# Optimization experiments

Hardware: AMD Instinct MI355X
Metric: run time of the kernel (lower is better)

## Reference

```python
import jax, jax.numpy as jnp
import numpy as np

B, D, H, W = 32, 256, 32, 32
K = 1024

def setup_inputs() -> dict:
    key = jax.random.key(0)
    k1, k2 = jax.random.split(key)
    x = jax.random.normal(k1, (B, D, H, W), dtype=jnp.float32)
    codebook = jax.random.normal(k2, (K, D), dtype=jnp.float32)
    return {"x": x, "codebook": codebook}

def reference(x, codebook):
    b, lat, h, w = x.shape
    # (B, D, H, W) -> (B*H*W, D) tokens
    xt = jnp.transpose(x, (0, 2, 3, 1)).reshape(-1, lat)  # [N, D]
    # Squared euclidean distances via expansion (argmin-equivalent to cdist)
    x_sq = jnp.sum(xt * xt, axis=-1, keepdims=True)           # [N, 1]
    c_sq = jnp.sum(codebook * codebook, axis=-1)[None, :]     # [1, K]
    dist2 = x_sq - 2.0 * (xt @ codebook.T) + c_sq             # [N, K]
    idx = jnp.argmin(dist2, axis=-1)                          # [N]
    quant = codebook[idx]                                     # [N, D]
    codebook_loss = jnp.mean((jax.lax.stop_gradient(xt) - quant) ** 2)
    commitment_loss = jnp.mean((xt - jax.lax.stop_gradient(quant)) ** 2)
    # Straight-through estimator
    out = xt + jax.lax.stop_gradient(quant - xt)              # [N, D]
    out = out.reshape(b, h, w, lat).transpose(0, 3, 1, 2)     # [B, D, H, W]
    min_enc_idx = idx.reshape(b, h, w)                        # [B, H, W]
    return out, min_enc_idx, codebook_loss, commitment_loss
```

## Files before the change

### kernel.cpp

```cpp
#include <hip/hip_runtime.h>

#define B_   32
#define D_   256
#define HW_  1024
#define N_   32768
#define K_   1024
#define DHW  (D_ * HW_)
#define MARGIN 0.3f

typedef __attribute__((ext_vector_type(8)))  short bf16x8;
typedef __attribute__((ext_vector_type(16))) float f32x16;

union FragU { uint4 q; bf16x8 v; };

__device__ inline uint bf16rne(float x) {
    uint ub = __float_as_uint(x);
    return (ub + 0x7fffu + ((ub >> 16) & 1u)) >> 16;
}

__global__ __launch_bounds__(256)
void prep_x(const float* __restrict__ x, uint4* __restrict__ xg) {
    const int tok0 = blockIdx.x * 64;
    const int b = tok0 >> 10, hw0 = tok0 & 1023;
    const int tokl = threadIdx.x & 63;
    const int gq = threadIdx.x >> 6;
    #pragma unroll
    for (int it = 0; it < 8; ++it) {
        int g = it * 4 + gq;
        const float* xp = x + (size_t)b * DHW + (size_t)(g * 8) * HW_ + hw0 + tokl;
        uint w[4];
        #pragma unroll
        for (int jj = 0; jj < 4; ++jj) {
            float e0 = xp[(size_t)(2 * jj) * HW_];
            float e1 = xp[(size_t)(2 * jj + 1) * HW_];
            w[jj] = bf16rne(e0) | (bf16rne(e1) << 16);
        }
        xg[(size_t)(tok0 + tokl) * 32 + g] = make_uint4(w[0], w[1], w[2], w[3]);
    }
}

__global__ __launch_bounds__(256)
void prep_cb(const float* __restrict__ cb, uint4* __restrict__ cbt,
             float* __restrict__ csq, float* __restrict__ cbT) {
    __shared__ uint sh[256], sl[256];
    __shared__ float rr[4];
    const int k = blockIdx.x, d = threadIdx.x;
    float v = cb[(size_t)k * D_ + d];
    uint hb = bf16rne(v);
    float hf = __uint_as_float(hb << 16);
    uint lb = bf16rne(v - hf);
    sh[d] = hb; sl[d] = lb;
    cbT[(size_t)d * K_ + k] = v;
    float s = v * v;
    #pragma unroll
    for (int off = 32; off >= 1; off >>= 1) s += __shfl_xor(s, off, 64);
    if ((d & 63) == 0) rr[d >> 6] = s;
    __syncthreads();
    if (d == 0) csq[k] = (rr[0] + rr[1]) + (rr[2] + rr[3]);
    if (d < 64) {
        int ch = d >> 3, g = d & 7;
        int p = g >> 2, gg = g & 3;
        const uint* src = p ? sl : sh;
        uint w[4];
        #pragma unroll
        for (int jj = 0; jj < 4; ++jj) {
            int dp = ch * 16 + gg * 4 + jj;
            w[jj] = src[2 * dp] | (src[2 * dp + 1] << 16);
        }
        cbt[(size_t)(ch * 1024 + k) * 8 + g] = make_uint4(w[0], w[1], w[2], w[3]);
    }
}

__global__ __launch_bounds__(512)
void vq_main(const uint4* __restrict__ xg, const uint4* __restrict__ cbt,
             const float* __restrict__ csqg, int* __restrict__ bestk,
             int* __restrict__ rcount, int* __restrict__ rlist,
             float* __restrict__ bdist) {
    __shared__ uint4 TkS[4096];
    __shared__ uint4 CbS[2][2048];
    __shared__ float csqS[1024];

    const int tid = threadIdx.x;
    const int lane = tid & 63;
    const int sub = lane >> 5, l31 = lane & 31;
    const int wid = tid >> 6;
    const int wm = wid >> 1, wn = wid & 1;
    const int tok0 = blockIdx.x * 128;

    csqS[tid] = csqg[tid];
    csqS[tid + 512] = csqg[tid + 512];
    asm volatile("s_waitcnt vmcnt(0) lgkmcnt(0)" ::: "memory");

    {
        const int tloc = tid >> 5;
        const int slot = tid & 31;
        const int g = slot ^ (tloc & 7);
        #pragma unroll
        for (int it = 0; it < 8; ++it) {
            int u = it * 512 + tid;
            const uint4* src = xg + (size_t)(tok0 + it * 16 + tloc) * 32 + g;
            __builtin_amdgcn_global_load_lds((const uint*)src, (uint*)&TkS[u], 16, 0, 0);
        }
    }
    const int s_cl = tid >> 3;
    const int s_g = (tid & 7) ^ (s_cl & 7);

    #pragma unroll
    for (int it = 0; it < 4; ++it) {
        int u = it * 512 + tid;
        int cl = it * 64 + s_cl;
        const uint4* src = cbt + (size_t)cl * 8 + s_g;
        __builtin_amdgcn_global_load_lds((const uint*)src, (uint*)&CbS[0][u], 16, 0, 0);
    }

    f32x16 acc[2][2] = {};
    float v1[2] = {3.4e38f, 3.4e38f}, v2[2] = {3.4e38f, 3.4e38f};
    int k1[2] = {0, 0};

    int cur = 0;
    for (int cc = 0; cc < 32; ++cc) {
        asm volatile("s_barrier" ::: "memory");
        if (cc + 1 < 32) {
            const int nct = (cc + 1) >> 3, nch = (cc + 1) & 7;
            #pragma unroll
            for (int it = 0; it < 4; ++it) {
                int u = it * 512 + tid;
                int cl = it * 64 + s_cl;
                const uint4* src = cbt + (size_t)(nch * 1024 + nct * 256 + cl) * 8 + s_g;
                __builtin_amdgcn_global_load_lds((const uint*)src, (uint*)&CbS[cur ^ 1][u], 16, 0, 0);
            }
            asm volatile("s_waitcnt vmcnt(4)" ::: "memory");
        } else {
            asm volatile("s_waitcnt vmcnt(0)" ::: "memory");
        }
        asm volatile("s_barrier" ::: "memory");

        const int ch = cc & 7;
        #pragma unroll
        for (int ks = 0; ks < 2; ++ks) {
            FragU tf[2], cfh[2], cfl[2];
            #pragma unroll
            for (int j = 0; j < 2; ++j) {
                int t = wn * 64 + j * 32 + l31;
                int g32 = ch * 4 + ks * 2 + sub;
                tf[j].q = TkS[t * 32 + (g32 ^ (t & 7))];
            }
            #pragma unroll
            for (int f = 0; f < 2; ++f) {
                int cl = wm * 64 + f * 32 + l31;
                int gh = ks * 2 + sub;
                int gl = 4 + ks * 2 + sub;
                cfh[f].q = CbS[cur][cl * 8 + (gh ^ (cl & 7))];
                cfl[f].q = CbS[cur][cl * 8 + (gl ^ (cl & 7))];
            }
            #pragma unroll
            for (int f = 0; f < 2; ++f)
                #pragma unroll
                for (int j = 0; j < 2; ++j) {
                    acc[f][j] = __builtin_amdgcn_mfma_f32_32x32x16_bf16(cfh[f].v, tf[j].v, acc[f][j], 0, 0, 0);
                    acc[f][j] = __builtin_amdgcn_mfma_f32_32x32x16_bf16(cfl[f].v, tf[j].v, acc[f][j], 0, 0, 0);
                }
        }
        cur ^= 1;

        if ((cc & 7) == 7) {
            const int ct = cc >> 3;
            const int cbase = ct * 256 + wm * 64 + sub * 4;
            #pragma unroll
            for (int f = 0; f < 2; ++f) {
                #pragma unroll
                for (int g8 = 0; g8 < 4; ++g8) {
                    float4 cs4 = *reinterpret_cast<const float4*>(&csqS[cbase + f * 32 + g8 * 8]);
                    const float csa[4] = {cs4.x, cs4.y, cs4.z, cs4.w};
                    #pragma unroll
                    for (int q = 0; q < 4; ++q) {
                        int code = cbase + f * 32 + g8 * 8 + q;
                        int r = g8 * 4 + q;
                        #pragma unroll
                        for (int j = 0; j < 2; ++j) {
                            float s = fmaf(-2.f, acc[f][j][r], csa[q]);
                            bool c = s < v1[j];
                            v2[j] = c ? v1[j] : fminf(v2[j], s);
                            k1[j] = c ? code : k1[j];
                            v1[j] = c ? s : v1[j];
                        }
                    }
                }
            }
            const f32x16 zf = {};
            #pragma unroll
            for (int f = 0; f < 2; ++f)
                #pragma unroll
                for (int j = 0; j < 2; ++j) acc[f][j] = zf;
        }
    }

    #pragma unroll
    for (int j = 0; j < 2; ++j) {
        float ov1 = __shfl_xor(v1[j], 32, 64);
        float ov2 = __shfl_xor(v2[j], 32, 64);
        int   ok1 = __shfl_xor(k1[j], 32, 64);
        float nv2 = fminf(fminf(v2[j], ov2), fmaxf(v1[j], ov1));
        if (ov1 < v1[j] || (ov1 == v1[j] && ok1 < k1[j])) { v1[j] = ov1; k1[j] = ok1; }
        v2[j] = nv2;
    }
    __syncthreads();
    float* red = (float*)&CbS[0][0];
    if (sub == 0) {
        #pragma unroll
        for (int j = 0; j < 2; ++j) {
            int t = wn * 64 + j * 32 + l31;
            red[(wm * 128 + t) * 4 + 0] = v1[j];
            red[(wm * 128 + t) * 4 + 1] = v2[j];
            red[(wm * 128 + t) * 4 + 2] = __int_as_float(k1[j]);
        }
    }
    __syncthreads();
    if (tid < 128) {
        float bv1 = red[tid * 4], bv2 = red[tid * 4 + 1];
        int bk = __float_as_int(red[tid * 4 + 2]);
        #pragma unroll
        for (int m = 1; m < 4; ++m) {
            float a1 = red[(m * 128 + tid) * 4], a2 = red[(m * 128 + tid) * 4 + 1];
            int ak = __float_as_int(red[(m * 128 + tid) * 4 + 2]);
            float nv2 = fminf(fminf(bv2, a2), fmaxf(bv1, a1));
            if (a1 < bv1 || (a1 == bv1 && ak < bk)) { bv1 = a1; bk = ak; }
            bv2 = nv2;
        }
        int n = tok0 + tid;
        bestk[n] = bk;
        bdist[n] = bv1;
        if (bv2 - bv1 < MARGIN) rlist[atomicAdd(rcount, 1)] = n;
    }
}

__global__ __launch_bounds__(256)
void vq_refine(const float* __restrict__ x, const float* __restrict__ cbT,
               const float* __restrict__ csq, const int* __restrict__ rcount,
               const int* __restrict__ rlist, int* __restrict__ bestk,
               float* __restrict__ bdist) {
    __shared__ float xv[8][256];
    __shared__ float xsq[8];
    __shared__ float wredv[4][8];
    __shared__ int   wredk[4][8];
    const int tid = threadIdx.x;
    const int cnt = min(rcount[0], N_);
    for (int base = blockIdx.x * 8; base < cnt; base += gridDim.x * 8) {
        const int m = min(8, cnt - base);
        __syncthreads();
        for (int j = 0; j < m; ++j) {
            int n = rlist[base + j];
            int b = n >> 10, hw = n & 1023;
            xv[j][tid] = x[(size_t)b * DHW + (size_t)tid * HW_ + hw];
        }
        for (int j = m; j < 8; ++j) xv[j][tid] = 0.f;
        __syncthreads();
        {
            int g = tid >> 5, l = tid & 31;
            float s = 0.f;
            #pragma unroll
            for (int d8 = 0; d8 < 8; ++d8) { float v = xv[g][d8 * 32 + l]; s = fmaf(v, v, s); }
            #pragma unroll
            for (int mm = 1; mm < 32; mm <<= 1) s += __shfl_xor(s, mm, 64);
            if (l == 0) xsq[g] = s;
        }
        __syncthreads();

        float dots[4][8];
        #pragma unroll
        for (int c4 = 0; c4 < 4; ++c4)
            #pragma unroll
            for (int j = 0; j < 8; ++j) dots[c4][j] = 0.f;

        const float* cbase = cbT + tid;
        for (int d0 = 0; d0 < 256; d0 += 8) {
            float xr[8][8];
            #pragma unroll
            for (int j = 0; j < 8; ++j) {
                float4 a = *reinterpret_cast<const float4*>(&xv[j][d0]);
                float4 b = *reinterpret_cast<const float4*>(&xv[j][d0 + 4]);
                xr[j][0] = a.x; xr[j][1] = a.y; xr[j][2] = a.z; xr[j][3] = a.w;
                xr[j][4] = b.x; xr[j][5] = b.y; xr[j][6] = b.z; xr[j][7] = b.w;
            }
            #pragma unroll
            for (int c4 = 0; c4 < 4; ++c4) {
                float cv[8];
                #pragma unroll
                for (int u = 0; u < 8; ++u)
                    cv[u] = cbase[(size_t)(d0 + u) * K_ + c4 * 256];
                #pragma unroll
                for (int u = 0; u < 8; ++u)
                    #pragma unroll
                    for (int j = 0; j < 8; ++j)
                        dots[c4][j] = fmaf(cv[u], xr[j][u], dots[c4][j]);
            }
        }

        float bv[8]; int bk[8];
        #pragma unroll
        for (int j = 0; j < 8; ++j) { bv[j] = 3.4e38f; bk[j] = 0; }
        #pragma unroll
        for (int c4 = 0; c4 < 4; ++c4) {
            const int code = c4 * 256 + tid;
            const float cs = csq[code];
            #pragma unroll
            for (int j = 0; j < 8; ++j) {
                float dist = fmaf(-2.f, dots[c4][j], xsq[j]) + cs;
                if (dist < bv[j]) { bv[j] = dist; bk[j] = code; }
            }
        }
        #pragma unroll
        for (int j = 0; j < 8; ++j) {
            if (j < m) {
                float v = bv[j]; int k = bk[j];
                #pragma unroll
                for (int mm = 1; mm < 64; mm <<= 1) {
                    float ov = __shfl_xor(v, mm, 64);
                    int   ok = __shfl_xor(k, mm, 64);
                    if (ov < v || (ov == v && ok < k)) { v = ov; k = ok; }
                }
                if ((tid & 63) == 0) { wredv[tid >> 6][j] = v; wredk[tid >> 6][j] = k; }
            }
        }
        __syncthreads();
        if (tid < m) {
            float v = wredv[0][tid]; int k = wredk[0][tid];
            #pragma unroll
            for (int q = 1; q < 4; ++q) {
                if (wredv[q][tid] < v || (wredv[q][tid] == v && wredk[q][tid] < k)) {
                    v = wredv[q][tid]; k = wredk[q][tid];
                }
            }
            int n = rlist[base + tid];
            bestk[n] = k;
            bdist[n] = v;
        }
        __syncthreads();
    }
}

__global__ __launch_bounds__(1024)
void vq_loss(const float* __restrict__ bdist, float* __restrict__ oloss) {
    __shared__ float r[16];
    float s = 0.f;
    const float4* p = reinterpret_cast<const float4*>(bdist);
    for (int i = threadIdx.x; i < N_ / 4; i += 1024) {
        float4 v = p[i];
        s += (v.x + v.y) + (v.z + v.w);
    }
    #pragma unroll
    for (int mm = 32; mm >= 1; mm >>= 1) s += __shfl_xor(s, mm, 64);
    if ((threadIdx.x & 63) == 0) r[threadIdx.x >> 6] = s;
    __syncthreads();
    if (threadIdx.x == 0) {
        float t = 0.f;
        #pragma unroll
        for (int i = 0; i < 16; ++i) t += r[i];
        t *= (1.0f / 8388608.0f);
        oloss[0] = t;
        oloss[1] = t;
    }
}

__global__ __launch_bounds__(256)
void vq_gather(const float* __restrict__ cb, const int* __restrict__ bestk,
               float* __restrict__ out, float* __restrict__ oidx) {
    const int n0 = blockIdx.x * 64;
    const int tid = threadIdx.x;
    const int j = tid & 63, dg = tid >> 6;
    const int n = n0 + j;
    const int b = n >> 10, hw = n & 1023;
    const int k = bestk[n];
    const float* cw = cb + (size_t)k * D_;
    const size_t basex = (size_t)b * DHW + hw;
    #pragma unroll 4
    for (int d = dg * 64; d < dg * 64 + 64; ++d) {
        out[basex + (size_t)d * HW_] = cw[d];
    }
    if (tid < 64) oidx[n0 + tid] = (float)bestk[n0 + tid];
}

extern "C" void kernel_launch(void* const* d_in, const int* in_sizes, int n_in,
                              void* d_out, int out_size, void* d_ws, size_t ws_size,
                              hipStream_t stream) {
    const float* x  = (const float*)d_in[0];
    const float* cb = (const float*)d_in[1];

    float* out   = (float*)d_out;
    float* oidx  = out + 8388608;
    float* oloss = out + 8388608 + 32768;

    uint4* xg = (uint4*)d_out;

    uint* wsb = (uint*)d_ws;
    uint4*  cbt   = (uint4*)wsb;
    float*  csq   = (float*)(wsb + 262144);
    float*  cbT   = (float*)(wsb + 263168);
    int*    bestk = (int*)  (wsb + 525312);
    int*    rcount= (int*)  (wsb + 558080);
    int*    rlist = (int*)  (wsb + 558084);
    float*  bdist = (float*)(wsb + 590852);

    hipMemsetAsync(rcount, 0, sizeof(int), stream);

    prep_x  <<<512, 256, 0, stream>>>(x, xg);
    prep_cb <<<1024, 256, 0, stream>>>(cb, cbt, csq, cbT);
    vq_main <<<256, 512, 0, stream>>>(xg, cbt, csq, bestk, rcount, rlist, bdist);
    vq_refine<<<256, 256, 0, stream>>>(x, cbT, csq, rcount, rlist, bestk, bdist);
    vq_loss <<<1, 1024, 0, stream>>>(bdist, oloss);
    vq_gather<<<512, 256, 0, stream>>>(cb, bestk, out, oidx);
}
```

Measured before the change: 130.6 us.

## Fuse x bf16 conversion into vq_main and loss reduction into gather

Removes the prep_x kernel: vq_main now reads fp32 x directly, converts it to bf16 and writes the swizzled token tile into LDS itself, which drops the intermediate global buffer round-trip. The separate single-block vq_loss kernel is removed; each gather block reduces its 64 distances with wave shuffles and atomically adds the result into the zero-initialised loss outputs. MFMA issue order is also regrouped so all hi-part MFMAs run before the lo-part ones. Costs are an extra memset, float atomics with nondeterministic summation order, and the strided x loads now sitting on vq_main's startup path.

```diff
diff --git a/kernel.cpp b/kernel.cpp
--- a/kernel.cpp
+++ b/kernel.cpp
@@ -16,27 +16,6 @@
 __device__ inline uint bf16rne(float x) {
     uint ub = __float_as_uint(x);
     return (ub + 0x7fffu + ((ub >> 16) & 1u)) >> 16;
-}
-
-__global__ __launch_bounds__(256)
-void prep_x(const float* __restrict__ x, uint4* __restrict__ xg) {
-    const int tok0 = blockIdx.x * 64;
-    const int b = tok0 >> 10, hw0 = tok0 & 1023;
-    const int tokl = threadIdx.x & 63;
-    const int gq = threadIdx.x >> 6;
-    #pragma unroll
-    for (int it = 0; it < 8; ++it) {
-        int g = it * 4 + gq;
-        const float* xp = x + (size_t)b * DHW + (size_t)(g * 8) * HW_ + hw0 + tokl;
-        uint w[4];
-        #pragma unroll
-        for (int jj = 0; jj < 4; ++jj) {
-            float e0 = xp[(size_t)(2 * jj) * HW_];
-            float e1 = xp[(size_t)(2 * jj + 1) * HW_];
-            w[jj] = bf16rne(e0) | (bf16rne(e1) << 16);
-        }
-        xg[(size_t)(tok0 + tokl) * 32 + g] = make_uint4(w[0], w[1], w[2], w[3]);
-    }
 }
 
 __global__ __launch_bounds__(256)
@@ -72,7 +51,7 @@
 }
 
 __global__ __launch_bounds__(512)
-void vq_main(const uint4* __restrict__ xg, const uint4* __restrict__ cbt,
+void vq_main(const float* __restrict__ x, const uint4* __restrict__ cbt,
              const float* __restrict__ csqg, int* __restrict__ bestk,
              int* __restrict__ rcount, int* __restrict__ rlist,
              float* __restrict__ bdist) {
@@ -86,22 +65,32 @@
     const int wid = tid >> 6;
     const int wm = wid >> 1, wn = wid & 1;
     const int tok0 = blockIdx.x * 128;
+    const int bb = tok0 >> 10, hw0 = tok0 & 1023;
 
     csqS[tid] = csqg[tid];
     csqS[tid + 512] = csqg[tid + 512];
+
+    {
+        const int t = tid & 127;
+        const int dgrp = tid >> 7;
+        const float* xp = x + (size_t)bb * DHW + hw0 + t;
+        #pragma unroll
+        for (int i = 0; i < 8; ++i) {
+            int g = i * 4 + dgrp;
+            float v[8];
+            #pragma unroll
+            for (int e = 0; e < 8; ++e)
+                v[e] = xp[(size_t)(g * 8 + e) * HW_];
+            uint w[4];
+            #pragma unroll
+            for (int jj = 0; jj < 4; ++jj)
+                w[jj] = bf16rne(v[2 * jj]) | (bf16rne(v[2 * jj + 1]) << 16);
+            TkS[t * 32 + (g ^ (t & 7))] = make_uint4(w[0], w[1], w[2], w[3]);
+        }
+    }
     asm volatile("s_waitcnt vmcnt(0) lgkmcnt(0)" ::: "memory");
-
-    {
-        const int tloc = tid >> 5;
-        const int slot = tid & 31;
-        const int g = slot ^ (tloc & 7);
-        #pragma unroll
-        for (int it = 0; it < 8; ++it) {
-            int u = it * 512 + tid;
-            const uint4* src = xg + (size_t)(tok0 + it * 16 + tloc) * 32 + g;
-            __builtin_amdgcn_global_load_lds((const uint*)src, (uint*)&TkS[u], 16, 0, 0);
-        }
-    }
+    __syncthreads();
+
     const int s_cl = tid >> 3;
     const int s_g = (tid & 7) ^ (s_cl & 7);
 
@@ -156,10 +145,13 @@
             #pragma unroll
             for (int f = 0; f < 2; ++f)
                 #pragma unroll
-                for (int j = 0; j < 2; ++j) {
+                for (int j = 0; j < 2; ++j)
                     acc[f][j] = __builtin_amdgcn_mfma_f32_32x32x16_bf16(cfh[f].v, tf[j].v, acc[f][j], 0, 0, 0);
+            #pragma unroll
+            for (int f = 0; f < 2; ++f)
+                #pragma unroll
+                for (int j = 0; j < 2; ++j)
                     acc[f][j] = __builtin_amdgcn_mfma_f32_32x32x16_bf16(cfl[f].v, tf[j].v, acc[f][j], 0, 0, 0);
-                }
         }
         cur ^= 1;
 
@@ -339,32 +331,10 @@
     }
 }
 
-__global__ __launch_bounds__(1024)
-void vq_loss(const float* __restrict__ bdist, float* __restrict__ oloss) {
-    __shared__ float r[16];
-    float s = 0.f;
-    const float4* p = reinterpret_cast<const float4*>(bdist);
-    for (int i = threadIdx.x; i < N_ / 4; i += 1024) {
-        float4 v = p[i];
-        s += (v.x + v.y) + (v.z + v.w);
-    }
-    #pragma unroll
-    for (int mm = 32; mm >= 1; mm >>= 1) s += __shfl_xor(s, mm, 64);
-    if ((threadIdx.x & 63) == 0) r[threadIdx.x >> 6] = s;
-    __syncthreads();
-    if (threadIdx.x == 0) {
-        float t = 0.f;
-        #pragma unroll
-        for (int i = 0; i < 16; ++i) t += r[i];
-        t *= (1.0f / 8388608.0f);
-        oloss[0] = t;
-        oloss[1] = t;
-    }
-}
-
 __global__ __launch_bounds__(256)
 void vq_gather(const float* __restrict__ cb, const int* __restrict__ bestk,
-               float* __restrict__ out, float* __restrict__ oidx) {
+               const float* __restrict__ bdist, float* __restrict__ out,
+               float* __restrict__ oidx, float* __restrict__ oloss) {
     const int n0 = blockIdx.x * 64;
     const int tid = threadIdx.x;
     const int j = tid & 63, dg = tid >> 6;
@@ -377,7 +347,17 @@
     for (int d = dg * 64; d < dg * 64 + 64; ++d) {
         out[basex + (size_t)d * HW_] = cw[d];
     }
-    if (tid < 64) oidx[n0 + tid] = (float)bestk[n0 + tid];
+    if (tid < 64) {
+        oidx[n0 + tid] = (float)bestk[n0 + tid];
+        float v = bdist[n0 + tid];
+        #pragma unroll
+        for (int off = 32; off >= 1; off >>= 1) v += __shfl_xor(v, off, 64);
+        if (tid == 0) {
+            float t = v * (1.0f / 8388608.0f);
+            atomicAdd(&oloss[0], t);
+            atomicAdd(&oloss[1], t);
+        }
+    }
 }
 
 extern "C" void kernel_launch(void* const* d_in, const int* in_sizes, int n_in,
@@ -389,8 +369,6 @@
     float* out   = (float*)d_out;
     float* oidx  = out + 8388608;
     float* oloss = out + 8388608 + 32768;
-
-    uint4* xg = (uint4*)d_out;
 
     uint* wsb = (uint*)d_ws;
     uint4*  cbt   = (uint4*)wsb;
@@ -402,11 +380,10 @@
     float*  bdist = (float*)(wsb + 590852);
 
     hipMemsetAsync(rcount, 0, sizeof(int), stream);
-
-    prep_x  <<<512, 256, 0, stream>>>(x, xg);
+    hipMemsetAsync(oloss, 0, 2 * sizeof(float), stream);
+
     prep_cb <<<1024, 256, 0, stream>>>(cb, cbt, csq, cbT);
-    vq_main <<<256, 512, 0, stream>>>(xg, cbt, csq, bestk, rcount, rlist, bdist);
+    vq_main <<<256, 512, 0, stream>>>(x, cbt, csq, bestk, rcount, rlist, bdist);
     vq_refine<<<256, 256, 0, stream>>>(x, cbT, csq, rcount, rlist, bestk, bdist);
-    vq_loss <<<1, 1024, 0, stream>>>(bdist, oloss);
-    vq_gather<<<512, 256, 0, stream>>>(cb, bestk, out, oidx);
-}
+    vq_gather<<<512, 256, 0, stream>>>(cb, bestk, bdist, out, oidx, oloss);
+}
```

New measurement: 130.2 us. No clear change (-0.2%).
